# Performance work log

Hardware: AMD Instinct MI355X
Metric: run time of the kernel (lower is better)

Reference implementation:

```python
import jax, jax.numpy as jnp
import numpy as np

B, T, D = 2, 2048, 768
K = 8          # ctm_iterations
M = 8          # ctm_memory_length
HID = 16       # ctm_memory_hidden
NS = 512       # ctm_n_synch


def _glu(a):
    h = a.shape[-1] // 2
    return a[..., :h] * jax.nn.sigmoid(a[..., h:])


def _ln(x, g, b):
    mu = jnp.mean(x, axis=-1, keepdims=True)
    var = jnp.mean((x - mu) ** 2, axis=-1, keepdims=True)
    return (x - mu) * jax.lax.rsqrt(var + 1e-5) * g + b


def setup_inputs() -> dict:
    key = jax.random.key(0)
    ks = jax.random.split(key, 10)
    s_syn = 1.0 / np.sqrt(2 * D)
    s1 = 1.0 / np.sqrt(M + 2 * HID)
    s2 = 1.0 / np.sqrt(HID + 2)
    return {
        "x": jax.random.normal(ks[0], (B, T, D), jnp.float32),
        "W_syn": jax.random.normal(ks[1], (2 * D, 2 * D), jnp.float32) * s_syn,
        "ln_g": jnp.ones((D,), jnp.float32),
        "ln_b": jnp.zeros((D,), jnp.float32),
        "w_nlm1": jax.random.uniform(ks[2], (M, 2 * HID, D), jnp.float32, -s1, s1),
        "b_nlm1": jnp.zeros((1, D, 2 * HID), jnp.float32),
        "w_nlm2": jax.random.uniform(ks[3], (HID, 2, D), jnp.float32, -s2, s2),
        "b_nlm2": jnp.zeros((1, D, 2), jnp.float32),
        "start_state": jax.random.normal(ks[4], (D,), jnp.float32),
        "start_trace": jax.random.normal(ks[5], (D, M), jnp.float32),
        "decay": jax.random.uniform(ks[6], (NS,), jnp.float32, 0.0, 3.0),
        "W_proj": jax.random.normal(ks[7], (D, NS), jnp.float32) / np.sqrt(NS),
        "synch_left": jax.random.randint(ks[8], (NS,), 0, D),
        "synch_right": jax.random.randint(ks[9], (NS,), 0, D),
    }


def reference(x, W_syn, ln_g, ln_b, w_nlm1, b_nlm1, w_nlm2, b_nlm2,
              start_state, start_trace, decay, W_proj, synch_left, synch_right):
    Bv, Tv, Dv = x.shape
    BT = Bv * Tv
    x_flat = x.reshape(BT, Dv)
    state0 = jnp.broadcast_to(start_state, (BT, Dv))
    trace0 = jnp.broadcast_to(start_trace, (BT, Dv, M))
    r = jnp.exp(-jnp.clip(decay, 0.0, 15.0))  # (NS,)
    alpha0 = jnp.zeros((BT, NS), x.dtype)
    beta0 = jnp.zeros((BT, NS), x.dtype)

    def step(carry, _):
        state, trace, alpha, beta = carry
        pre = jnp.concatenate([x_flat, state], axis=-1)            # (BT, 2D)
        new_state = _ln(_glu(pre @ W_syn.T), ln_g, ln_b)            # (BT, D)
        trace = jnp.concatenate([trace[:, :, 1:], new_state[:, :, None]], axis=-1)  # (BT, D, M)
        h = _glu(jnp.einsum('bnm,mon->bno', trace, w_nlm1) + b_nlm1)  # (BT, D, HID)
        state = _glu(jnp.einsum('bnm,mon->bno', h, w_nlm2) + b_nlm2)[..., 0]  # (BT, D)
        pp = state[:, synch_left] * state[:, synch_right]           # (BT, NS)
        alpha = r * alpha + pp
        beta = r * beta + 1.0
        return (state, trace, alpha, beta), None

    (state, trace, alpha, beta), _ = jax.lax.scan(
        step, (state0, trace0, alpha0, beta0), None, length=K)
    synch = alpha / jnp.sqrt(beta)                                  # (BT, NS)
    return (synch @ W_proj.T).reshape(Bv, Tv, Dv)
```

## Files before the change

kernel.cpp:

```cpp
#include <hip/hip_runtime.h>
#include <math.h>

#define BT_TOTAL 4096
#define DD 768
#define TWOD 1536
#define M_MEM 8
#define NHID 16
#define NSY 512
#define K_ITER 8

typedef unsigned short u16;
typedef __attribute__((ext_vector_type(8))) __bf16 bf16x8;
typedef __attribute__((ext_vector_type(4))) float f32x4;

__device__ __forceinline__ float sigmoidf_(float x) {
    return 1.0f / (1.0f + __expf(-x));
}

__device__ __forceinline__ u16 f2bf(float f) {
    unsigned int u = __float_as_uint(f);
    unsigned int r = (u + 0x7FFFu + ((u >> 16) & 1u)) >> 16;
    return (u16)r;
}
__device__ __forceinline__ float bf2f(u16 h) {
    return __uint_as_float(((unsigned int)h) << 16);
}

__device__ __forceinline__ void gload_lds16(const void* g, void* l) {
    __builtin_amdgcn_global_load_lds(
        (const __attribute__((address_space(1))) unsigned int*)g,
        (__attribute__((address_space(3))) unsigned int*)l,
        16, 0, 0);
}

__global__ __launch_bounds__(256)
void init_kernel(u16* __restrict__ shi, u16* __restrict__ slo,
                 float* __restrict__ alpha, const float* __restrict__ start_state) {
    int idx = blockIdx.x * 256 + threadIdx.x;
    const int nstate = BT_TOTAL * DD;
    if (idx < nstate) {
        float a = start_state[idx % DD];
        u16 h = f2bf(a);
        shi[idx] = h;
        slo[idx] = f2bf(a - bf2f(h));
    } else {
        int a = idx - nstate;
        if (a < BT_TOTAL * NSY) alpha[a] = 0.0f;
    }
}

__global__ __launch_bounds__(256)
void split_w_kernel(const float* __restrict__ W,
                    u16* __restrict__ wxhi, u16* __restrict__ wxlo,
                    u16* __restrict__ wshi, u16* __restrict__ wslo) {
    int idx = blockIdx.x * 256 + threadIdx.x;
    int j = idx / DD, k = idx % DD;
    float a = W[(size_t)j * TWOD + k];
    float b = W[(size_t)j * TWOD + DD + k];
    u16 ha = f2bf(a); wxhi[idx] = ha; wxlo[idx] = f2bf(a - bf2f(ha));
    u16 hb = f2bf(b); wshi[idx] = hb; wslo[idx] = f2bf(b - bf2f(hb));
}

__global__ __launch_bounds__(256)
void split_x_kernel(const float* __restrict__ x,
                    u16* __restrict__ xhi, u16* __restrict__ xlo) {
    int idx = blockIdx.x * 256 + threadIdx.x;
    float a = x[idx];
    u16 h = f2bf(a);
    xhi[idx] = h;
    xlo[idx] = f2bf(a - bf2f(h));
}

__global__ __launch_bounds__(256)
void scale_wproj_kernel(const float* __restrict__ wproj,
                        const float* __restrict__ decay,
                        float* __restrict__ wps) {
    int idx = blockIdx.x * 256 + threadIdx.x;
    int s = idx & (NSY - 1);
    float dcl = fminf(fmaxf(decay[s], 0.0f), 15.0f);
    float r = __expf(-dcl);
    float beta = 1.0f, rp = r;
    #pragma unroll
    for (int i = 1; i < K_ITER; ++i) { beta += rp; rp *= r; }
    wps[idx] = wproj[idx] * rsqrtf(beta);
}

#define TM 128
#define TN 128
#define TK 64

__global__ __launch_bounds__(256)
void gemm_mfma_split(const u16* __restrict__ Ahi, const u16* __restrict__ Alo,
                     const u16* __restrict__ Bhi, const u16* __restrict__ Blo,
                     const float* __restrict__ C0,
                     float* __restrict__ C, int ldc) {
    __shared__ u16 sAh[TM * TK];
    __shared__ u16 sAl[TM * TK];
    __shared__ u16 sBh[TN * TK];
    __shared__ u16 sBl[TN * TK];
    const int tid  = threadIdx.x;
    const int w    = tid >> 6;
    const int lane = tid & 63;
    const int row0 = blockIdx.y * TM;
    const int col0 = blockIdx.x * TN;
    const int wr = (w >> 1) * 64;
    const int wc = (w & 1) * 64;

    const f32x4 zero = {0.f, 0.f, 0.f, 0.f};
    f32x4 acc[4][4];
    #pragma unroll
    for (int i = 0; i < 4; ++i)
        #pragma unroll
        for (int j = 0; j < 4; ++j) acc[i][j] = zero;

    const int lr = lane >> 3;
    const int ls = lane & 7;

    for (int kt = 0; kt < DD; kt += TK) {
        __syncthreads();
        #pragma unroll
        for (int g = 0; g < 4; ++g) {
            int r  = w * 32 + g * 8 + lr;
            int ss = ls ^ (r & 7);
            size_t goffA = (size_t)(row0 + r) * DD + kt + ss * 8;
            size_t goffB = (size_t)(col0 + r) * DD + kt + ss * 8;
            int lo = (w * 32 + g * 8) * TK;
            gload_lds16(Ahi + goffA, &sAh[lo]);
            gload_lds16(Alo + goffA, &sAl[lo]);
            gload_lds16(Bhi + goffB, &sBh[lo]);
            gload_lds16(Blo + goffB, &sBl[lo]);
        }
        __syncthreads();
        #pragma unroll
        for (int ks = 0; ks < 2; ++ks) {
            bf16x8 ah[4], al[4], bh[4], bl[4];
            #pragma unroll
            for (int f = 0; f < 4; ++f) {
                int ra = wr + f * 16 + (lane & 15);
                int sa = (ks * 4 + (lane >> 4)) ^ (ra & 7);
                ah[f] = *(const bf16x8*)(const void*)(sAh + ra * TK + sa * 8);
                al[f] = *(const bf16x8*)(const void*)(sAl + ra * TK + sa * 8);
                int rb = wc + f * 16 + (lane & 15);
                int sb = (ks * 4 + (lane >> 4)) ^ (rb & 7);
                bh[f] = *(const bf16x8*)(const void*)(sBh + rb * TK + sb * 8);
                bl[f] = *(const bf16x8*)(const void*)(sBl + rb * TK + sb * 8);
            }
            #pragma unroll
            for (int i = 0; i < 4; ++i)
                #pragma unroll
                for (int j = 0; j < 4; ++j) {
                    acc[i][j] = __builtin_amdgcn_mfma_f32_16x16x32_bf16(ah[i], bh[j], acc[i][j], 0, 0, 0);
                    acc[i][j] = __builtin_amdgcn_mfma_f32_16x16x32_bf16(ah[i], bl[j], acc[i][j], 0, 0, 0);
                    acc[i][j] = __builtin_amdgcn_mfma_f32_16x16x32_bf16(al[i], bh[j], acc[i][j], 0, 0, 0);
                }
        }
    }

    const int cc = lane & 15;
    const int rr = (lane >> 4) * 4;
    #pragma unroll
    for (int i = 0; i < 4; ++i) {
        #pragma unroll
        for (int j = 0; j < 4; ++j) {
            int gr = row0 + wr + i * 16 + rr;
            int gc = col0 + wc + j * 16 + cc;
            #pragma unroll
            for (int q = 0; q < 4; ++q) {
                size_t off = (size_t)(gr + q) * ldc + gc;
                float v = acc[i][j][q];
                if (C0) v += C0[off];
                C[off] = v;
            }
        }
    }
}

#define GBM 128
#define GBN 128
#define GBK 16

__global__ __launch_bounds__(256)
void gemm_abT(const float* __restrict__ A, int lda,
              const float* __restrict__ B, int ldb,
              const float* __restrict__ C0,
              float* __restrict__ C, int ldc, int K) {
    __shared__ float As[GBK][GBM + 4];
    __shared__ float Bs[GBK][GBN + 4];
    const int tid = threadIdx.x;
    const int tx = tid & 15, ty = tid >> 4;
    const int row0 = blockIdx.y * GBM;
    const int col0 = blockIdx.x * GBN;
    const int lr = tid >> 2;
    const int lk = (tid & 3) << 2;

    float acc[8][8];
    #pragma unroll
    for (int i = 0; i < 8; ++i)
        #pragma unroll
        for (int j = 0; j < 8; ++j) acc[i][j] = 0.0f;

    const float* Ap  = A + (size_t)(row0 + lr) * lda + lk;
    const float* Ap2 = A + (size_t)(row0 + lr + 64) * lda + lk;
    const float* Bp  = B + (size_t)(col0 + lr) * ldb + lk;
    const float* Bp2 = B + (size_t)(col0 + lr + 64) * ldb + lk;

    for (int kt = 0; kt < K; kt += GBK) {
        float4 av0 = *(const float4*)(Ap  + kt);
        float4 av1 = *(const float4*)(Ap2 + kt);
        float4 bv0 = *(const float4*)(Bp  + kt);
        float4 bv1 = *(const float4*)(Bp2 + kt);
        __syncthreads();
        As[lk+0][lr] = av0.x; As[lk+1][lr] = av0.y; As[lk+2][lr] = av0.z; As[lk+3][lr] = av0.w;
        As[lk+0][lr+64] = av1.x; As[lk+1][lr+64] = av1.y; As[lk+2][lr+64] = av1.z; As[lk+3][lr+64] = av1.w;
        Bs[lk+0][lr] = bv0.x; Bs[lk+1][lr] = bv0.y; Bs[lk+2][lr] = bv0.z; Bs[lk+3][lr] = bv0.w;
        Bs[lk+0][lr+64] = bv1.x; Bs[lk+1][lr+64] = bv1.y; Bs[lk+2][lr+64] = bv1.z; Bs[lk+3][lr+64] = bv1.w;
        __syncthreads();
        #pragma unroll
        for (int kk = 0; kk < GBK; ++kk) {
            float a[8], b[8];
            *(float4*)&a[0] = *(const float4*)&As[kk][ty * 8];
            *(float4*)&a[4] = *(const float4*)&As[kk][ty * 8 + 4];
            *(float4*)&b[0] = *(const float4*)&Bs[kk][tx * 8];
            *(float4*)&b[4] = *(const float4*)&Bs[kk][tx * 8 + 4];
            #pragma unroll
            for (int i = 0; i < 8; ++i)
                #pragma unroll
                for (int j = 0; j < 8; ++j)
                    acc[i][j] = fmaf(a[i], b[j], acc[i][j]);
        }
    }

    #pragma unroll
    for (int i = 0; i < 8; ++i) {
        size_t roff = (size_t)(row0 + ty * 8 + i) * ldc + col0 + tx * 8;
        float o[8];
        #pragma unroll
        for (int j = 0; j < 8; ++j) o[j] = acc[i][j];
        if (C0) {
            #pragma unroll
            for (int j = 0; j < 8; ++j) o[j] += C0[roff + j];
        }
        *(float4*)(C + roff)     = *(const float4*)&o[0];
        *(float4*)(C + roff + 4) = *(const float4*)&o[4];
    }
}

__global__ __launch_bounds__(256)
void glu_ln_kernel(const float* __restrict__ act,
                   const float* __restrict__ ln_g, const float* __restrict__ ln_b,
                   float* __restrict__ ns_out) {
    int wave = threadIdx.x >> 6;
    int lane = threadIdx.x & 63;
    int row = blockIdx.x * 4 + wave;
    const float* arow = act + (size_t)row * TWOD;
    float g[12];
    float s = 0.0f, ss = 0.0f;
    #pragma unroll
    for (int q = 0; q < 12; ++q) {
        int c = lane + q * 64;
        float a = arow[c];
        float b = arow[c + DD];
        float v = a * sigmoidf_(b);
        g[q] = v; s += v; ss += v * v;
    }
    #pragma unroll
    for (int off = 32; off; off >>= 1) {
        s  += __shfl_xor(s, off);
        ss += __shfl_xor(ss, off);
    }
    float mu  = s * (1.0f / 768.0f);
    float var = ss * (1.0f / 768.0f) - mu * mu;
    float rstd = rsqrtf(var + 1e-5f);
    float* orow = ns_out + (size_t)row * DD;
    #pragma unroll
    for (int q = 0; q < 12; ++q) {
        int c = lane + q * 64;
        orow[c] = (g[q] - mu) * rstd * ln_g[c] + ln_b[c];
    }
}

#define NC 32
#define RT 32

__global__ __launch_bounds__(256)
void nlm_kernel(const float* __restrict__ ns_hist, const float* __restrict__ st,
                const float* __restrict__ w1, const float* __restrict__ b1,
                const float* __restrict__ w2, const float* __restrict__ b2,
                u16* __restrict__ shi, u16* __restrict__ slo, int k) {
    __shared__ float w1s[M_MEM][32][NC];
    __shared__ float w2s[NHID][2][NC];
    __shared__ float b1s[NC][33];
    __shared__ float b2s[NC][3];
    __shared__ float sts[NC][9];
    const int tid = threadIdx.x;
    const int n0 = blockIdx.x * NC;
    const int r0 = blockIdx.y * RT;

    for (int idx = tid; idx < M_MEM * 32 * NC; idx += 256) {
        int mo = idx / NC, nl = idx % NC;
        ((float*)w1s)[idx] = w1[(size_t)mo * DD + n0 + nl];
    }
    for (int idx = tid; idx < NHID * 2 * NC; idx += 256) {
        int mo = idx / NC, nl = idx % NC;
        ((float*)w2s)[idx] = w2[(size_t)mo * DD + n0 + nl];
    }
    for (int idx = tid; idx < NC * 32; idx += 256) {
        int nl = idx >> 5, o = idx & 31;
        b1s[nl][o] = b1[(size_t)(n0 + nl) * 32 + o];
    }
    if (tid < NC * 2) { int nl = tid >> 1, o = tid & 1; b2s[nl][o] = b2[(size_t)(n0 + nl) * 2 + o]; }
    if (tid < NC * 8) { int nl = tid >> 3, m = tid & 7; sts[nl][m] = st[(size_t)(n0 + nl) * 8 + m]; }
    __syncthreads();

    const int nl = tid & (NC - 1);
    const int n = n0 + nl;
    const int rbase = r0 + (tid >> 5);

    #pragma unroll
    for (int ri = 0; ri < 4; ++ri) {
        int row = rbase + ri * 8;
        float t[M_MEM];
        #pragma unroll
        for (int m = 0; m < M_MEM; ++m) {
            if (m < 7 - k)
                t[m] = sts[nl][m + k + 1];
            else
                t[m] = ns_hist[(size_t)(m - 7 + k) * (BT_TOTAL * DD) + (size_t)row * DD + n];
        }
        float h[NHID];
        #pragma unroll
        for (int o = 0; o < NHID; ++o) {
            float pa = b1s[nl][o], pb = b1s[nl][o + 16];
            #pragma unroll
            for (int m = 0; m < M_MEM; ++m) {
                pa = fmaf(t[m], w1s[m][o][nl], pa);
                pb = fmaf(t[m], w1s[m][o + 16][nl], pb);
            }
            h[o] = pa * sigmoidf_(pb);
        }
        float p0 = b2s[nl][0], p1 = b2s[nl][1];
        #pragma unroll
        for (int m = 0; m < NHID; ++m) {
            p0 = fmaf(h[m], w2s[m][0][nl], p0);
            p1 = fmaf(h[m], w2s[m][1][nl], p1);
        }
        float v = p0 * sigmoidf_(p1);
        size_t off = (size_t)row * DD + n;
        u16 hv = f2bf(v);
        shi[off] = hv;
        slo[off] = f2bf(v - bf2f(hv));
    }
}

__global__ __launch_bounds__(256)
void pp_kernel(const u16* __restrict__ shi, const u16* __restrict__ slo,
               const float* __restrict__ decay,
               const int* __restrict__ sl, const int* __restrict__ sr,
               float* __restrict__ alpha) {
    __shared__ float srow[4][DD];
    int wave = threadIdx.x >> 6, lane = threadIdx.x & 63;
    int row = blockIdx.x * 4 + wave;
    size_t base = (size_t)row * DD;
    #pragma unroll
    for (int q = 0; q < 12; ++q) {
        int c = lane + q * 64;
        srow[wave][c] = bf2f(shi[base + c]) + bf2f(slo[base + c]);
    }
    __syncthreads();
    float* arow = alpha + (size_t)row * NSY;
    #pragma unroll
    for (int q = 0; q < 8; ++q) {
        int s = lane + q * 64;
        float dcl = fminf(fmaxf(decay[s], 0.0f), 15.0f);
        float r = __expf(-dcl);
        float pp = srow[wave][sl[s]] * srow[wave][sr[s]];
        arow[s] = r * arow[s] + pp;
    }
}

extern "C" void kernel_launch(void* const* d_in, const int* in_sizes, int n_in,
                              void* d_out, int out_size, void* d_ws, size_t ws_size,
                              hipStream_t stream) {
    const float* x        = (const float*)d_in[0];
    const float* W_syn    = (const float*)d_in[1];
    const float* ln_g     = (const float*)d_in[2];
    const float* ln_b     = (const float*)d_in[3];
    const float* w1       = (const float*)d_in[4];
    const float* b1       = (const float*)d_in[5];
    const float* w2       = (const float*)d_in[6];
    const float* b2       = (const float*)d_in[7];
    const float* start_st = (const float*)d_in[8];
    const float* start_tr = (const float*)d_in[9];
    const float* decay    = (const float*)d_in[10];
    const float* W_proj   = (const float*)d_in[11];
    const int*   sl       = (const int*)d_in[12];
    const int*   sr       = (const int*)d_in[13];
    float* out = (float*)d_out;

    float* ws    = (float*)d_ws;
    float* xpre  = ws;
    float* act   = xpre  + (size_t)BT_TOTAL * TWOD;
    float* nsh   = act   + (size_t)BT_TOTAL * TWOD;
    float* alpha = nsh   + (size_t)K_ITER * BT_TOTAL * DD;
    float* wps   = alpha + (size_t)BT_TOTAL * NSY;
    u16* u16base = (u16*)(wps + (size_t)DD * NSY);
    u16* xhi  = u16base;
    u16* xlo  = xhi  + (size_t)BT_TOTAL * DD;
    u16* shi  = xlo  + (size_t)BT_TOTAL * DD;
    u16* slo  = shi  + (size_t)BT_TOTAL * DD;
    u16* wxhi = slo  + (size_t)BT_TOTAL * DD;
    u16* wxlo = wxhi + (size_t)TWOD * DD;
    u16* wshi = wxlo + (size_t)TWOD * DD;
    u16* wslo = wshi + (size_t)TWOD * DD;

    {
        int total = BT_TOTAL * (DD + NSY);
        init_kernel<<<(total + 255) / 256, 256, 0, stream>>>(shi, slo, alpha, start_st);
    }
    split_w_kernel<<<(TWOD * DD) / 256, 256, 0, stream>>>(W_syn, wxhi, wxlo, wshi, wslo);
    split_x_kernel<<<(BT_TOTAL * DD) / 256, 256, 0, stream>>>(x, xhi, xlo);
    scale_wproj_kernel<<<(DD * NSY) / 256, 256, 0, stream>>>(W_proj, decay, wps);

    {
        dim3 g(TWOD / TN, BT_TOTAL / TM);
        gemm_mfma_split<<<g, 256, 0, stream>>>(xhi, xlo, wxhi, wxlo, nullptr, xpre, TWOD);
    }

    for (int k = 0; k < K_ITER; ++k) {
        dim3 g(TWOD / TN, BT_TOTAL / TM);
        gemm_mfma_split<<<g, 256, 0, stream>>>(shi, slo, wshi, wslo, xpre, act, TWOD);
        glu_ln_kernel<<<BT_TOTAL / 4, 256, 0, stream>>>(act, ln_g, ln_b,
                                                        nsh + (size_t)k * BT_TOTAL * DD);
        dim3 gn(DD / NC, BT_TOTAL / RT);
        nlm_kernel<<<gn, 256, 0, stream>>>(nsh, start_tr, w1, b1, w2, b2, shi, slo, k);
        pp_kernel<<<BT_TOTAL / 4, 256, 0, stream>>>(shi, slo, decay, sl, sr, alpha);
    }

    {
        dim3 g(DD / GBN, BT_TOTAL / GBM);
        gemm_abT<<<g, 256, 0, stream>>>(alpha, NSY, wps, NSY, nullptr, out, DD, NSY);
    }
}
```

Baseline: 1.293 ms.

## Run final projection on split-bf16 MFMA GEMM and restructure NLM loop over rows

The final alpha×W_proj projection moves from a scalar fp32 FMA GEMM to the split-bf16 MFMA GEMM, with new kernels that split alpha and the scaled W_proj into hi/lo bf16 parts, and the GEMM now takes leading-dimension and K parameters. Separately, the NLM kernel is reordered so each hidden unit's weights are loaded from LDS once and reused across four rows instead of being reloaded per row. This trades an extra split pass and more register pressure in the NLM kernel for tensor-core throughput and fewer LDS reads.

```diff
diff --git a/kernel.cpp b/kernel.cpp
--- a/kernel.cpp
+++ b/kernel.cpp
@@ -74,7 +74,7 @@
 __global__ __launch_bounds__(256)
 void scale_wproj_kernel(const float* __restrict__ wproj,
                         const float* __restrict__ decay,
-                        float* __restrict__ wps) {
+                        u16* __restrict__ wpshi, u16* __restrict__ wpslo) {
     int idx = blockIdx.x * 256 + threadIdx.x;
     int s = idx & (NSY - 1);
     float dcl = fminf(fmaxf(decay[s], 0.0f), 15.0f);
@@ -82,7 +82,20 @@
     float beta = 1.0f, rp = r;
     #pragma unroll
     for (int i = 1; i < K_ITER; ++i) { beta += rp; rp *= r; }
-    wps[idx] = wproj[idx] * rsqrtf(beta);
+    float w = wproj[idx] * rsqrtf(beta);
+    u16 h = f2bf(w);
+    wpshi[idx] = h;
+    wpslo[idx] = f2bf(w - bf2f(h));
+}
+
+__global__ __launch_bounds__(256)
+void split_alpha_kernel(const float* __restrict__ alpha,
+                        u16* __restrict__ ahi, u16* __restrict__ alo) {
+    int idx = blockIdx.x * 256 + threadIdx.x;
+    float a = alpha[idx];
+    u16 h = f2bf(a);
+    ahi[idx] = h;
+    alo[idx] = f2bf(a - bf2f(h));
 }
 
 #define TM 128
@@ -93,7 +106,7 @@
 void gemm_mfma_split(const u16* __restrict__ Ahi, const u16* __restrict__ Alo,
                      const u16* __restrict__ Bhi, const u16* __restrict__ Blo,
                      const float* __restrict__ C0,
-                     float* __restrict__ C, int ldc) {
+                     float* __restrict__ C, int ldc, int ldab, int Kdim) {
     __shared__ u16 sAh[TM * TK];
     __shared__ u16 sAl[TM * TK];
     __shared__ u16 sBh[TN * TK];
@@ -116,14 +129,14 @@
     const int lr = lane >> 3;
     const int ls = lane & 7;
 
-    for (int kt = 0; kt < DD; kt += TK) {
+    for (int kt = 0; kt < Kdim; kt += TK) {
         __syncthreads();
         #pragma unroll
         for (int g = 0; g < 4; ++g) {
             int r  = w * 32 + g * 8 + lr;
             int ss = ls ^ (r & 7);
-            size_t goffA = (size_t)(row0 + r) * DD + kt + ss * 8;
-            size_t goffB = (size_t)(col0 + r) * DD + kt + ss * 8;
+            size_t goffA = (size_t)(row0 + r) * ldab + kt + ss * 8;
+            size_t goffB = (size_t)(col0 + r) * ldab + kt + ss * 8;
             int lo = (w * 32 + g * 8) * TK;
             gload_lds16(Ahi + goffA, &sAh[lo]);
             gload_lds16(Alo + goffA, &sAl[lo]);
@@ -175,76 +188,6 @@
     }
 }
 
-#define GBM 128
-#define GBN 128
-#define GBK 16
-
-__global__ __launch_bounds__(256)
-void gemm_abT(const float* __restrict__ A, int lda,
-              const float* __restrict__ B, int ldb,
-              const float* __restrict__ C0,
-              float* __restrict__ C, int ldc, int K) {
-    __shared__ float As[GBK][GBM + 4];
-    __shared__ float Bs[GBK][GBN + 4];
-    const int tid = threadIdx.x;
-    const int tx = tid & 15, ty = tid >> 4;
-    const int row0 = blockIdx.y * GBM;
-    const int col0 = blockIdx.x * GBN;
-    const int lr = tid >> 2;
-    const int lk = (tid & 3) << 2;
-
-    float acc[8][8];
-    #pragma unroll
-    for (int i = 0; i < 8; ++i)
-        #pragma unroll
-        for (int j = 0; j < 8; ++j) acc[i][j] = 0.0f;
-
-    const float* Ap  = A + (size_t)(row0 + lr) * lda + lk;
-    const float* Ap2 = A + (size_t)(row0 + lr + 64) * lda + lk;
-    const float* Bp  = B + (size_t)(col0 + lr) * ldb + lk;
-    const float* Bp2 = B + (size_t)(col0 + lr + 64) * ldb + lk;
-
-    for (int kt = 0; kt < K; kt += GBK) {
-        float4 av0 = *(const float4*)(Ap  + kt);
-        float4 av1 = *(const float4*)(Ap2 + kt);
-        float4 bv0 = *(const float4*)(Bp  + kt);
-        float4 bv1 = *(const float4*)(Bp2 + kt);
-        __syncthreads();
-        As[lk+0][lr] = av0.x; As[lk+1][lr] = av0.y; As[lk+2][lr] = av0.z; As[lk+3][lr] = av0.w;
-        As[lk+0][lr+64] = av1.x; As[lk+1][lr+64] = av1.y; As[lk+2][lr+64] = av1.z; As[lk+3][lr+64] = av1.w;
-        Bs[lk+0][lr] = bv0.x; Bs[lk+1][lr] = bv0.y; Bs[lk+2][lr] = bv0.z; Bs[lk+3][lr] = bv0.w;
-        Bs[lk+0][lr+64] = bv1.x; Bs[lk+1][lr+64] = bv1.y; Bs[lk+2][lr+64] = bv1.z; Bs[lk+3][lr+64] = bv1.w;
-        __syncthreads();
-        #pragma unroll
-        for (int kk = 0; kk < GBK; ++kk) {
-            float a[8], b[8];
-            *(float4*)&a[0] = *(const float4*)&As[kk][ty * 8];
-            *(float4*)&a[4] = *(const float4*)&As[kk][ty * 8 + 4];
-            *(float4*)&b[0] = *(const float4*)&Bs[kk][tx * 8];
-            *(float4*)&b[4] = *(const float4*)&Bs[kk][tx * 8 + 4];
-            #pragma unroll
-            for (int i = 0; i < 8; ++i)
-                #pragma unroll
-                for (int j = 0; j < 8; ++j)
-                    acc[i][j] = fmaf(a[i], b[j], acc[i][j]);
-        }
-    }
-
-    #pragma unroll
-    for (int i = 0; i < 8; ++i) {
-        size_t roff = (size_t)(row0 + ty * 8 + i) * ldc + col0 + tx * 8;
-        float o[8];
-        #pragma unroll
-        for (int j = 0; j < 8; ++j) o[j] = acc[i][j];
-        if (C0) {
-            #pragma unroll
-            for (int j = 0; j < 8; ++j) o[j] += C0[roff + j];
-        }
-        *(float4*)(C + roff)     = *(const float4*)&o[0];
-        *(float4*)(C + roff + 4) = *(const float4*)&o[4];
-    }
-}
-
 __global__ __launch_bounds__(256)
 void glu_ln_kernel(const float* __restrict__ act,
                    const float* __restrict__ ln_g, const float* __restrict__ ln_b,
@@ -316,35 +259,51 @@
     const int n = n0 + nl;
     const int rbase = r0 + (tid >> 5);
 
+    float t[4][M_MEM];
     #pragma unroll
     for (int ri = 0; ri < 4; ++ri) {
         int row = rbase + ri * 8;
-        float t[M_MEM];
         #pragma unroll
         for (int m = 0; m < M_MEM; ++m) {
             if (m < 7 - k)
-                t[m] = sts[nl][m + k + 1];
+                t[ri][m] = sts[nl][m + k + 1];
             else
-                t[m] = ns_hist[(size_t)(m - 7 + k) * (BT_TOTAL * DD) + (size_t)row * DD + n];
-        }
-        float h[NHID];
-        #pragma unroll
-        for (int o = 0; o < NHID; ++o) {
-            float pa = b1s[nl][o], pb = b1s[nl][o + 16];
+                t[ri][m] = ns_hist[(size_t)(m - 7 + k) * (BT_TOTAL * DD) + (size_t)row * DD + n];
+        }
+    }
+
+    float p0[4], p1[4];
+    #pragma unroll
+    for (int ri = 0; ri < 4; ++ri) { p0[ri] = b2s[nl][0]; p1[ri] = b2s[nl][1]; }
+
+    #pragma unroll
+    for (int o = 0; o < NHID; ++o) {
+        float wa[M_MEM], wb[M_MEM];
+        #pragma unroll
+        for (int m = 0; m < M_MEM; ++m) {
+            wa[m] = w1s[m][o][nl];
+            wb[m] = w1s[m][o + 16][nl];
+        }
+        float w20 = w2s[o][0][nl], w21 = w2s[o][1][nl];
+        float ba = b1s[nl][o], bb = b1s[nl][o + 16];
+        #pragma unroll
+        for (int ri = 0; ri < 4; ++ri) {
+            float pa = ba, pb = bb;
             #pragma unroll
             for (int m = 0; m < M_MEM; ++m) {
-                pa = fmaf(t[m], w1s[m][o][nl], pa);
-                pb = fmaf(t[m], w1s[m][o + 16][nl], pb);
+                pa = fmaf(t[ri][m], wa[m], pa);
+                pb = fmaf(t[ri][m], wb[m], pb);
             }
-            h[o] = pa * sigmoidf_(pb);
-        }
-        float p0 = b2s[nl][0], p1 = b2s[nl][1];
-        #pragma unroll
-        for (int m = 0; m < NHID; ++m) {
-            p0 = fmaf(h[m], w2s[m][0][nl], p0);
-            p1 = fmaf(h[m], w2s[m][1][nl], p1);
-        }
-        float v = p0 * sigmoidf_(p1);
+            float h = pa * sigmoidf_(pb);
+            p0[ri] = fmaf(h, w20, p0[ri]);
+            p1[ri] = fmaf(h, w21, p1[ri]);
+        }
+    }
+
+    #pragma unroll
+    for (int ri = 0; ri < 4; ++ri) {
+        int row = rbase + ri * 8;
+        float v = p0[ri] * sigmoidf_(p1[ri]);
         size_t off = (size_t)row * DD + n;
         u16 hv = f2bf(v);
         shi[off] = hv;
@@ -402,16 +361,19 @@
     float* act   = xpre  + (size_t)BT_TOTAL * TWOD;
     float* nsh   = act   + (size_t)BT_TOTAL * TWOD;
     float* alpha = nsh   + (size_t)K_ITER * BT_TOTAL * DD;
-    float* wps   = alpha + (size_t)BT_TOTAL * NSY;
-    u16* u16base = (u16*)(wps + (size_t)DD * NSY);
-    u16* xhi  = u16base;
-    u16* xlo  = xhi  + (size_t)BT_TOTAL * DD;
-    u16* shi  = xlo  + (size_t)BT_TOTAL * DD;
-    u16* slo  = shi  + (size_t)BT_TOTAL * DD;
-    u16* wxhi = slo  + (size_t)BT_TOTAL * DD;
-    u16* wxlo = wxhi + (size_t)TWOD * DD;
-    u16* wshi = wxlo + (size_t)TWOD * DD;
-    u16* wslo = wshi + (size_t)TWOD * DD;
+    u16* u16base = (u16*)(alpha + (size_t)BT_TOTAL * NSY);
+    u16* xhi   = u16base;
+    u16* xlo   = xhi   + (size_t)BT_TOTAL * DD;
+    u16* shi   = xlo   + (size_t)BT_TOTAL * DD;
+    u16* slo   = shi   + (size_t)BT_TOTAL * DD;
+    u16* wxhi  = slo   + (size_t)BT_TOTAL * DD;
+    u16* wxlo  = wxhi  + (size_t)TWOD * DD;
+    u16* wshi  = wxlo  + (size_t)TWOD * DD;
+    u16* wslo  = wshi  + (size_t)TWOD * DD;
+    u16* wpshi = wslo  + (size_t)TWOD * DD;
+    u16* wpslo = wpshi + (size_t)DD * NSY;
+    u16* ahi   = wpslo + (size_t)DD * NSY;
+    u16* alo   = ahi   + (size_t)BT_TOTAL * NSY;
 
     {
         int total = BT_TOTAL * (DD + NSY);
@@ -419,16 +381,16 @@
     }
     split_w_kernel<<<(TWOD * DD) / 256, 256, 0, stream>>>(W_syn, wxhi, wxlo, wshi, wslo);
     split_x_kernel<<<(BT_TOTAL * DD) / 256, 256, 0, stream>>>(x, xhi, xlo);
-    scale_wproj_kernel<<<(DD * NSY) / 256, 256, 0, stream>>>(W_proj, decay, wps);
+    scale_wproj_kernel<<<(DD * NSY) / 256, 256, 0, stream>>>(W_proj, decay, wpshi, wpslo);
 
     {
         dim3 g(TWOD / TN, BT_TOTAL / TM);
-        gemm_mfma_split<<<g, 256, 0, stream>>>(xhi, xlo, wxhi, wxlo, nullptr, xpre, TWOD);
+        gemm_mfma_split<<<g, 256, 0, stream>>>(xhi, xlo, wxhi, wxlo, nullptr, xpre, TWOD, DD, DD);
     }
 
     for (int k = 0; k < K_ITER; ++k) {
         dim3 g(TWOD / TN, BT_TOTAL / TM);
-        gemm_mfma_split<<<g, 256, 0, stream>>>(shi, slo, wshi, wslo, xpre, act, TWOD);
+        gemm_mfma_split<<<g, 256, 0, stream>>>(shi, slo, wshi, wslo, xpre, act, TWOD, DD, DD);
         glu_ln_kernel<<<BT_TOTAL / 4, 256, 0, stream>>>(act, ln_g, ln_b,
                                                         nsh + (size_t)k * BT_TOTAL * DD);
         dim3 gn(DD / NC, BT_TOTAL / RT);
@@ -436,8 +398,9 @@
         pp_kernel<<<BT_TOTAL / 4, 256, 0, stream>>>(shi, slo, decay, sl, sr, alpha);
     }
 
+    split_alpha_kernel<<<(BT_TOTAL * NSY) / 256, 256, 0, stream>>>(alpha, ahi, alo);
     {
-        dim3 g(DD / GBN, BT_TOTAL / GBM);
-        gemm_abT<<<g, 256, 0, stream>>>(alpha, NSY, wps, NSY, nullptr, out, DD, NSY);
-    }
-}
+        dim3 g(DD / TN, BT_TOTAL / TM);
+        gemm_mfma_split<<<g, 256, 0, stream>>>(ahi, alo, wpshi, wpslo, nullptr, out, DD, NSY, NSY);
+    }
+}
```

Measured after the change: 1.138 ms. 12.0% less time.
